# Kernel tuning notes

Measured on AMD Instinct MI355X. Metric: run time of the kernel, lower is better.

The kernel has to match this reference:

```python
import jax, jax.numpy as jnp
import numpy as np

B, D_IN, N, K, L, D_OUT = 64, 1024, 50000, 32, 3, 256


def setup_inputs() -> dict:
    key = jax.random.key(0)
    k = jax.random.split(key, 7)
    x = jax.random.normal(k[0], (B, D_IN), dtype=jnp.float32)
    W0 = jax.random.normal(k[1], (N, D_IN), dtype=jnp.float32) * 0.02
    b0 = jax.random.normal(k[2], (N,), dtype=jnp.float32) * 0.02
    Wv = jax.random.normal(k[3], (L, N, K), dtype=jnp.float32) * 0.1
    Wout = jax.random.normal(k[4], (D_OUT, N), dtype=jnp.float32) * 0.02
    bout = jax.random.normal(k[5], (D_OUT,), dtype=jnp.float32) * 0.02
    src = jax.random.randint(k[6], (L, N, K), 0, N, dtype=jnp.int64)
    return {"x": x, "W0": W0, "b0": b0, "Wv": Wv, "Wout": Wout, "bout": bout, "src": src}


def reference(x, W0, b0, Wv, Wout, bout, src):
    # layer 0: dense input->sources, relu, transpose -> [N, B]
    h = jax.nn.relu(x @ W0.T + b0).T

    # each hidden layer: per-vertex gather of K source activations + 1xK matmul + relu
    def step(h_prev, layer):
        w, s = layer                      # w: [N, K], s: [N, K]
        gathered = h_prev[s]              # [N, K, B] irregular gather
        h_new = jax.nn.relu(jnp.einsum('nk,nkb->nb', w, gathered))
        return h_new, None

    h, _ = jax.lax.scan(step, h, (Wv, src))

    # last layer -> output Linear (the module's _linear_dummy)
    return h.T @ Wout.T + bout            # [B, D_OUT]
```

## Files before the change

kernel.cpp:

```cpp
#include <hip/hip_runtime.h>

#define NV 50000
#define NVP 50176
#define BDIM 64
#define DIN 1024
#define KFAN 32
#define DOUT 256
#define KSTEPS (DIN / 32)
#define XPK_N (KSTEPS * 512)
#define OPC_CHUNK 128
#define OPC_NCH (NVP / OPC_CHUNK)

typedef short bf16x8 __attribute__((ext_vector_type(8)));
typedef float f32x4 __attribute__((ext_vector_type(4)));

__device__ __forceinline__ unsigned short bf16_rtn(float f) {
  unsigned u = __float_as_uint(f);
  return (unsigned short)((u + 0x7fffu + ((u >> 16) & 1u)) >> 16);
}
__device__ __forceinline__ float bf16_to_f(unsigned short v) {
  return __uint_as_float(((unsigned)v) << 16);
}
__device__ __forceinline__ void gload_lds16(const void* g, void* l) {
  __builtin_amdgcn_global_load_lds(
      (const __attribute__((address_space(1))) void*)g,
      (__attribute__((address_space(3))) void*)l, 16, 0, 0);
}

__global__ __launch_bounds__(256) void pack_x(const float* __restrict__ x,
                                              uint4* __restrict__ xpk8) {
  int tid = blockIdx.x * 256 + threadIdx.x;
  int ks = tid >> 8;
  int g = (tid >> 6) & 3;
  int l = tid & 63;
  int b = g * 16 + (l & 15);
  int k0 = ks * 32 + (l >> 4) * 8;
  unsigned hi[8], lo[8];
#pragma unroll
  for (int j = 0; j < 8; ++j) {
    float f = x[b * DIN + k0 + j];
    unsigned u = __float_as_uint(f);
    hi[j] = u >> 16;
    float fh = __uint_as_float(u & 0xffff0000u);
    lo[j] = bf16_rtn(f - fh);
  }
  uint4 vh, vl;
  vh.x = hi[0] | (hi[1] << 16); vh.y = hi[2] | (hi[3] << 16);
  vh.z = hi[4] | (hi[5] << 16); vh.w = hi[6] | (hi[7] << 16);
  vl.x = lo[0] | (lo[1] << 16); vl.y = lo[2] | (lo[3] << 16);
  vl.z = lo[4] | (lo[5] << 16); vl.w = lo[6] | (lo[7] << 16);
  int idx = (ks * 4 + g) * 128 + l;
#pragma unroll
  for (int c = 0; c < 8; ++c) {
    xpk8[(size_t)c * XPK_N + idx] = vh;
    xpk8[(size_t)c * XPK_N + idx + 64] = vl;
  }
}

__global__ __launch_bounds__(256) void layer0_mfma(
    const float* __restrict__ W0, const float* __restrict__ b0,
    const uint4* __restrict__ xpk8, unsigned short* __restrict__ h)
{
  __shared__ float wlds[2][64 * 32];
  __shared__ uint4 xlds[2][512];
  const int t = threadIdx.x;
  const int lane = t & 63;
  const int w = t >> 6;
  const int rq = lane >> 4;
  const int rr = lane & 15;
  const int n0 = blockIdx.x * 64;
  const uint4* xsrc = xpk8 + (size_t)(blockIdx.x & 7) * XPK_N;

  int s_row[2], s_srcg[2];
#pragma unroll
  for (int p = 0; p < 2; ++p) {
    int flat = p * 256 + t;
    s_row[p] = flat >> 3;
    s_srcg[p] = (flat & 7) ^ (s_row[p] & 7);
  }
  int rowg0 = n0 + s_row[0]; if (rowg0 > NV - 1) rowg0 = NV - 1;
  int rowg1 = n0 + s_row[1]; if (rowg1 > NV - 1) rowg1 = NV - 1;
  const float* sp0 = W0 + (size_t)rowg0 * DIN + s_srcg[0] * 4;
  const float* sp1 = W0 + (size_t)rowg1 * DIN + s_srcg[1] * 4;

  const int myrow = w * 16 + rr;
  const int sw = (myrow & 7) << 4;
  const int off0 = (myrow * 128 + ((rq * 32) ^ sw)) >> 2;
  const int off1 = (myrow * 128 + ((rq * 32 + 16) ^ sw)) >> 2;

  f32x4 acc[4];
#pragma unroll
  for (int g = 0; g < 4; ++g) acc[g] = (f32x4){0.f, 0.f, 0.f, 0.f};

  gload_lds16(sp0, &wlds[0][(0 * 256 + t) * 4]);
  gload_lds16(sp1, &wlds[0][(1 * 256 + t) * 4]);
  gload_lds16(xsrc + (0 * 256 + t), &xlds[0][0 * 256 + t]);
  gload_lds16(xsrc + (1 * 256 + t), &xlds[0][1 * 256 + t]);
  __syncthreads();

  for (int ks = 0; ks < KSTEPS; ++ks) {
    const int cur = ks & 1;
    if (ks + 1 < KSTEPS) {
      const int ko = (ks + 1) * 32;
      gload_lds16(sp0 + ko, &wlds[cur ^ 1][(0 * 256 + t) * 4]);
      gload_lds16(sp1 + ko, &wlds[cur ^ 1][(1 * 256 + t) * 4]);
      const uint4* xs = xsrc + (ks + 1) * 512;
      gload_lds16(xs + (0 * 256 + t), &xlds[cur ^ 1][0 * 256 + t]);
      gload_lds16(xs + (1 * 256 + t), &xlds[cur ^ 1][1 * 256 + t]);
    }
    uint4 xc[4][2];
#pragma unroll
    for (int g = 0; g < 4; ++g) {
      xc[g][0] = xlds[cur][g * 128 + lane];
      xc[g][1] = xlds[cur][g * 128 + 64 + lane];
    }
    const float* wb = &wlds[cur][0];
    float4 wv0 = *(const float4*)(wb + off0);
    float4 wv1 = *(const float4*)(wb + off1);
    bf16x8 whi, wlo;
    {
      float wf[8] = {wv0.x, wv0.y, wv0.z, wv0.w, wv1.x, wv1.y, wv1.z, wv1.w};
#pragma unroll
      for (int e = 0; e < 8; ++e) {
        unsigned u = __float_as_uint(wf[e]);
        whi[e] = (short)(u >> 16);
        float l = wf[e] - __uint_as_float(u & 0xffff0000u);
        wlo[e] = (short)bf16_rtn(l);
      }
    }
#pragma unroll
    for (int g = 0; g < 4; ++g) {
      bf16x8 xh = __builtin_bit_cast(bf16x8, xc[g][0]);
      bf16x8 xl = __builtin_bit_cast(bf16x8, xc[g][1]);
      acc[g] = __builtin_amdgcn_mfma_f32_16x16x32_bf16(whi, xh, acc[g], 0, 0, 0);
      acc[g] = __builtin_amdgcn_mfma_f32_16x16x32_bf16(wlo, xh, acc[g], 0, 0, 0);
      acc[g] = __builtin_amdgcn_mfma_f32_16x16x32_bf16(whi, xl, acc[g], 0, 0, 0);
    }
    __syncthreads();
  }

#pragma unroll
  for (int r = 0; r < 4; ++r) {
    int n = n0 + w * 16 + rq * 4 + r;
    if (n < NV) {
      float bias = b0[n];
#pragma unroll
      for (int g = 0; g < 4; ++g) {
        float v = fmaxf(acc[g][r] + bias, 0.f);
        h[(size_t)n * BDIM + g * 16 + rr] = bf16_rtn(v);
      }
    }
  }
}

__global__ __launch_bounds__(256) void sparse_layer(
    const unsigned short* __restrict__ hin, const float* __restrict__ wv,
    const int* __restrict__ src, unsigned short* __restrict__ hout)
{
  const int lane = threadIdx.x & 63;
  int n = blockIdx.x * 4 + (threadIdx.x >> 6);
  n = __builtin_amdgcn_readfirstlane(n);
  const float* wrow = wv + (size_t)n * KFAN;
  const int* srow = src + (size_t)n * KFAN;
  float acc = 0.f;
#pragma unroll
  for (int k = 0; k < KFAN; ++k) {
    int s = srow[k];
    float w = wrow[k];
    acc = fmaf(w, bf16_to_f(hin[(size_t)s * BDIM + lane]), acc);
  }
  hout[(size_t)n * BDIM + lane] = bf16_rtn(fmaxf(acc, 0.f));
}

__global__ __launch_bounds__(256) void transpose_h(
    const unsigned short* __restrict__ h, unsigned short* __restrict__ hT)
{
  const int lane = threadIdx.x & 63;
  const int wv = threadIdx.x >> 6;
  const int n0 = (blockIdx.x * 4 + wv) * 8;
  unsigned short v[8];
#pragma unroll
  for (int i = 0; i < 8; ++i) {
    int n = n0 + i;
    v[i] = (n < NV) ? h[(size_t)n * BDIM + lane] : (unsigned short)0;
  }
  uint4 o;
  o.x = v[0] | ((unsigned)v[1] << 16);
  o.y = v[2] | ((unsigned)v[3] << 16);
  o.z = v[4] | ((unsigned)v[5] << 16);
  o.w = v[6] | ((unsigned)v[7] << 16);
  *(uint4*)(hT + (size_t)lane * NVP + n0) = o;
}

__global__ __launch_bounds__(64) void out_partial_mfma(
    const unsigned short* __restrict__ hT, const float* __restrict__ Wout,
    float* __restrict__ part)
{
  const int lane = threadIdx.x;
  const int rq = lane >> 4;
  const int rr = lane & 15;
  const int dtile = blockIdx.x;
  const int chunk = blockIdx.y;

  f32x4 acc[4][4];
#pragma unroll
  for (int f = 0; f < 4; ++f)
#pragma unroll
    for (int g = 0; g < 4; ++g) acc[f][g] = (f32x4){0.f, 0.f, 0.f, 0.f};

#pragma unroll
  for (int ks = 0; ks < OPC_CHUNK / 32; ++ks) {
    const int n0 = chunk * OPC_CHUNK + ks * 32 + rq * 8;
    bf16x8 hb[4];
#pragma unroll
    for (int g = 0; g < 4; ++g)
      hb[g] = *(const bf16x8*)(hT + (size_t)(g * 16 + rr) * NVP + n0);
    int nb = n0 > (NV - 8) ? (NV - 8) : n0;
#pragma unroll
    for (int f = 0; f < 4; ++f) {
      const float* wp = Wout + (size_t)(dtile * 64 + f * 16 + rr) * NV + nb;
      float4 a0 = *(const float4*)(wp);
      float4 a1 = *(const float4*)(wp + 4);
      float wf[8] = {a0.x, a0.y, a0.z, a0.w, a1.x, a1.y, a1.z, a1.w};
      bf16x8 whi, wlo;
#pragma unroll
      for (int e = 0; e < 8; ++e) {
        unsigned u = __float_as_uint(wf[e]);
        whi[e] = (short)(u >> 16);
        float l = wf[e] - __uint_as_float(u & 0xffff0000u);
        wlo[e] = (short)bf16_rtn(l);
      }
#pragma unroll
      for (int g = 0; g < 4; ++g) {
        acc[f][g] = __builtin_amdgcn_mfma_f32_16x16x32_bf16(whi, hb[g], acc[f][g], 0, 0, 0);
        acc[f][g] = __builtin_amdgcn_mfma_f32_16x16x32_bf16(wlo, hb[g], acc[f][g], 0, 0, 0);
      }
    }
  }
  float* pbase = part + ((size_t)dtile * OPC_NCH + chunk) * 4096;
#pragma unroll
  for (int f = 0; f < 4; ++f)
#pragma unroll
    for (int g = 0; g < 4; ++g)
#pragma unroll
      for (int r = 0; r < 4; ++r)
        pbase[(f * 16 + rq * 4 + r) * 64 + g * 16 + rr] = acc[f][g][r];
}

__global__ __launch_bounds__(256) void out_reduce(
    const float* __restrict__ part, const float* __restrict__ bout,
    float* __restrict__ out)
{
  int tid = blockIdx.x * 256 + threadIdx.x;
  int b = tid & 63;
  int d = tid >> 6;
  int dtile = d >> 6;
  int dd = d & 63;
  float s = bout[d];
  for (int c = 0; c < OPC_NCH; ++c)
    s += part[((size_t)dtile * OPC_NCH + c) * 4096 + dd * 64 + b];
  out[(size_t)b * DOUT + d] = s;
}

extern "C" void kernel_launch(void* const* d_in, const int* in_sizes, int n_in,
                              void* d_out, int out_size, void* d_ws, size_t ws_size,
                              hipStream_t stream)
{
  const float* x    = (const float*)d_in[0];
  const float* W0   = (const float*)d_in[1];
  const float* b0   = (const float*)d_in[2];
  const float* Wv   = (const float*)d_in[3];
  const float* Wout = (const float*)d_in[4];
  const float* bout = (const float*)d_in[5];
  const int*   src  = (const int*)d_in[6];
  float* out = (float*)d_out;

  char* ws = (char*)d_ws;
  const size_t hbf = (size_t)NV * BDIM * 2;
  const size_t hTb = (size_t)NVP * BDIM * 2;
  const size_t xpkb = (size_t)8 * XPK_N * 16;
  unsigned short* hb0 = (unsigned short*)ws;
  unsigned short* hb1 = (unsigned short*)(ws + hbf);
  unsigned short* hT  = (unsigned short*)(ws + 2 * hbf);
  uint4* xpk8 = (uint4*)(ws + 2 * hbf + hTb);
  float* part = (float*)(ws + 2 * hbf + hTb + xpkb);

  pack_x<<<32, 256, 0, stream>>>(x, xpk8);
  layer0_mfma<<<(NV + 63) / 64, 256, 0, stream>>>(W0, b0, xpk8, hb0);

  const size_t lstride = (size_t)NV * KFAN;
  sparse_layer<<<NV / 4, 256, 0, stream>>>(hb0, Wv, src, hb1);
  sparse_layer<<<NV / 4, 256, 0, stream>>>(hb1, Wv + lstride, src + lstride, hb0);
  sparse_layer<<<NV / 4, 256, 0, stream>>>(hb0, Wv + 2 * lstride, src + 2 * lstride, hb1);

  transpose_h<<<NVP / 32, 256, 0, stream>>>(hb1, hT);
  out_partial_mfma<<<dim3(4, OPC_NCH), 64, 0, stream>>>(hT, Wout, part);
  out_reduce<<<(BDIM * DOUT) / 256, 256, 0, stream>>>(part, bout, out);
}
```

Measured before the change: 185.8 us.

## Triple-buffer layer0 LDS staging with partial vmcnt waits

Replaces the double-buffered global-to-LDS pipeline in the dense layer-0 MFMA kernel with a three-stage ring that prefetches two K-steps ahead. Each step waits only for the oldest batch of loads (vmcnt(4)) rather than draining all of them through __syncthreads, so global loads can stay in flight during compute. This uses more LDS, which may lower occupancy, and it depends on hand-written waitcnt and barrier placement being correct.

```diff
diff --git a/kernel.cpp b/kernel.cpp
--- a/kernel.cpp
+++ b/kernel.cpp
@@ -61,8 +61,8 @@
     const float* __restrict__ W0, const float* __restrict__ b0,
     const uint4* __restrict__ xpk8, unsigned short* __restrict__ h)
 {
-  __shared__ float wlds[2][64 * 32];
-  __shared__ uint4 xlds[2][512];
+  __shared__ float wlds[3][64 * 32];
+  __shared__ uint4 xlds[3][512];
   const int t = threadIdx.x;
   const int lane = t & 63;
   const int w = t >> 6;
@@ -88,31 +88,38 @@
   const int off0 = (myrow * 128 + ((rq * 32) ^ sw)) >> 2;
   const int off1 = (myrow * 128 + ((rq * 32 + 16) ^ sw)) >> 2;
 
+  auto stage = [&](int ks, int buf) {
+    const int ko = ks * 32;
+    gload_lds16(sp0 + ko, &wlds[buf][(0 * 256 + t) * 4]);
+    gload_lds16(sp1 + ko, &wlds[buf][(1 * 256 + t) * 4]);
+    const uint4* xs = xsrc + ks * 512;
+    gload_lds16(xs + (0 * 256 + t), &xlds[buf][0 * 256 + t]);
+    gload_lds16(xs + (1 * 256 + t), &xlds[buf][1 * 256 + t]);
+  };
+
   f32x4 acc[4];
 #pragma unroll
   for (int g = 0; g < 4; ++g) acc[g] = (f32x4){0.f, 0.f, 0.f, 0.f};
 
-  gload_lds16(sp0, &wlds[0][(0 * 256 + t) * 4]);
-  gload_lds16(sp1, &wlds[0][(1 * 256 + t) * 4]);
-  gload_lds16(xsrc + (0 * 256 + t), &xlds[0][0 * 256 + t]);
-  gload_lds16(xsrc + (1 * 256 + t), &xlds[0][1 * 256 + t]);
-  __syncthreads();
-
+  stage(0, 0);
+  stage(1, 1);
+  asm volatile("s_waitcnt vmcnt(4)" ::: "memory");
+  __builtin_amdgcn_sched_barrier(0);
+  __builtin_amdgcn_s_barrier();
+
+  int cur = 0;
   for (int ks = 0; ks < KSTEPS; ++ks) {
-    const int cur = ks & 1;
-    if (ks + 1 < KSTEPS) {
-      const int ko = (ks + 1) * 32;
-      gload_lds16(sp0 + ko, &wlds[cur ^ 1][(0 * 256 + t) * 4]);
-      gload_lds16(sp1 + ko, &wlds[cur ^ 1][(1 * 256 + t) * 4]);
-      const uint4* xs = xsrc + (ks + 1) * 512;
-      gload_lds16(xs + (0 * 256 + t), &xlds[cur ^ 1][0 * 256 + t]);
-      gload_lds16(xs + (1 * 256 + t), &xlds[cur ^ 1][1 * 256 + t]);
-    }
+    if (ks + 2 < KSTEPS) {
+      int nb = cur + 2; if (nb >= 3) nb -= 3;
+      stage(ks + 2, nb);
+      __builtin_amdgcn_sched_barrier(0);
+    }
+    const uint4* xb = &xlds[cur][0];
     uint4 xc[4][2];
 #pragma unroll
     for (int g = 0; g < 4; ++g) {
-      xc[g][0] = xlds[cur][g * 128 + lane];
-      xc[g][1] = xlds[cur][g * 128 + 64 + lane];
+      xc[g][0] = xb[g * 128 + lane];
+      xc[g][1] = xb[g * 128 + 64 + lane];
     }
     const float* wb = &wlds[cur][0];
     float4 wv0 = *(const float4*)(wb + off0);
@@ -136,7 +143,16 @@
       acc[g] = __builtin_amdgcn_mfma_f32_16x16x32_bf16(wlo, xh, acc[g], 0, 0, 0);
       acc[g] = __builtin_amdgcn_mfma_f32_16x16x32_bf16(whi, xl, acc[g], 0, 0, 0);
     }
-    __syncthreads();
+    if (ks + 2 < KSTEPS) {
+      asm volatile("s_waitcnt vmcnt(4)" ::: "memory");
+      __builtin_amdgcn_sched_barrier(0);
+      __builtin_amdgcn_s_barrier();
+    } else if (ks + 1 < KSTEPS) {
+      asm volatile("s_waitcnt vmcnt(0)" ::: "memory");
+      __builtin_amdgcn_sched_barrier(0);
+      __builtin_amdgcn_s_barrier();
+    }
+    cur = (cur == 2) ? 0 : cur + 1;
   }
 
 #pragma unroll
```

Measured after the change: 205.5 us. +10.6%, slower.

## Deepen layer-0 W0 staging to 128-column chunks and read x from global

Applied to the files above, without the earlier changes.

The layer-0 GEMM now stages W0 through LDS in larger 128-column chunks, eight per row tile, using a wider XOR swizzle. Loads are issued two stages ahead with explicit vmcnt waits and barriers, replacing the old per-32-column double buffer. The packed x operand is no longer copied into LDS; each wave reads it straight from global memory, relying on cache hits. This cuts the number of barriers and keeps more W0 bytes in flight, but uses more LDS per block, which can lower occupancy, and adds global-load latency for x inside the MFMA loop.

```diff
diff --git a/kernel.cpp b/kernel.cpp
--- a/kernel.cpp
+++ b/kernel.cpp
@@ -61,8 +61,7 @@
     const float* __restrict__ W0, const float* __restrict__ b0,
     const uint4* __restrict__ xpk8, unsigned short* __restrict__ h)
 {
-  __shared__ float wlds[2][64 * 32];
-  __shared__ uint4 xlds[2][512];
+  __shared__ float wlds[2][64 * 128];
   const int t = threadIdx.x;
   const int lane = t & 63;
   const int w = t >> 6;
@@ -71,72 +70,73 @@
   const int n0 = blockIdx.x * 64;
   const uint4* xsrc = xpk8 + (size_t)(blockIdx.x & 7) * XPK_N;
 
-  int s_row[2], s_srcg[2];
-#pragma unroll
-  for (int p = 0; p < 2; ++p) {
-    int flat = p * 256 + t;
-    s_row[p] = flat >> 3;
-    s_srcg[p] = (flat & 7) ^ (s_row[p] & 7);
-  }
-  int rowg0 = n0 + s_row[0]; if (rowg0 > NV - 1) rowg0 = NV - 1;
-  int rowg1 = n0 + s_row[1]; if (rowg1 > NV - 1) rowg1 = NV - 1;
-  const float* sp0 = W0 + (size_t)rowg0 * DIN + s_srcg[0] * 4;
-  const float* sp1 = W0 + (size_t)rowg1 * DIN + s_srcg[1] * 4;
+  const float* sp[8];
+#pragma unroll
+  for (int p = 0; p < 8; ++p) {
+    int f = p * 256 + t;
+    int row = f >> 5;
+    int su = (f & 31) ^ (row & 31);
+    int rg = n0 + row; if (rg > NV - 1) rg = NV - 1;
+    sp[p] = W0 + (size_t)rg * DIN + su * 4;
+  }
+  auto stage = [&](int ss, int buf) {
+    const int co = ss * 128;
+#pragma unroll
+    for (int p = 0; p < 8; ++p)
+      gload_lds16(sp[p] + co, &wlds[buf][(p * 256 + t) * 4]);
+  };
 
   const int myrow = w * 16 + rr;
-  const int sw = (myrow & 7) << 4;
-  const int off0 = (myrow * 128 + ((rq * 32) ^ sw)) >> 2;
-  const int off1 = (myrow * 128 + ((rq * 32 + 16) ^ sw)) >> 2;
+  const int rowbase = myrow * 128;
+  const int swz = myrow & 31;
 
   f32x4 acc[4];
 #pragma unroll
   for (int g = 0; g < 4; ++g) acc[g] = (f32x4){0.f, 0.f, 0.f, 0.f};
 
-  gload_lds16(sp0, &wlds[0][(0 * 256 + t) * 4]);
-  gload_lds16(sp1, &wlds[0][(1 * 256 + t) * 4]);
-  gload_lds16(xsrc + (0 * 256 + t), &xlds[0][0 * 256 + t]);
-  gload_lds16(xsrc + (1 * 256 + t), &xlds[0][1 * 256 + t]);
-  __syncthreads();
-
-  for (int ks = 0; ks < KSTEPS; ++ks) {
-    const int cur = ks & 1;
-    if (ks + 1 < KSTEPS) {
-      const int ko = (ks + 1) * 32;
-      gload_lds16(sp0 + ko, &wlds[cur ^ 1][(0 * 256 + t) * 4]);
-      gload_lds16(sp1 + ko, &wlds[cur ^ 1][(1 * 256 + t) * 4]);
-      const uint4* xs = xsrc + (ks + 1) * 512;
-      gload_lds16(xs + (0 * 256 + t), &xlds[cur ^ 1][0 * 256 + t]);
-      gload_lds16(xs + (1 * 256 + t), &xlds[cur ^ 1][1 * 256 + t]);
-    }
-    uint4 xc[4][2];
-#pragma unroll
-    for (int g = 0; g < 4; ++g) {
-      xc[g][0] = xlds[cur][g * 128 + lane];
-      xc[g][1] = xlds[cur][g * 128 + 64 + lane];
-    }
-    const float* wb = &wlds[cur][0];
-    float4 wv0 = *(const float4*)(wb + off0);
-    float4 wv1 = *(const float4*)(wb + off1);
-    bf16x8 whi, wlo;
-    {
-      float wf[8] = {wv0.x, wv0.y, wv0.z, wv0.w, wv1.x, wv1.y, wv1.z, wv1.w};
-#pragma unroll
-      for (int e = 0; e < 8; ++e) {
-        unsigned u = __float_as_uint(wf[e]);
-        whi[e] = (short)(u >> 16);
-        float l = wf[e] - __uint_as_float(u & 0xffff0000u);
-        wlo[e] = (short)bf16_rtn(l);
-      }
-    }
-#pragma unroll
-    for (int g = 0; g < 4; ++g) {
-      bf16x8 xh = __builtin_bit_cast(bf16x8, xc[g][0]);
-      bf16x8 xl = __builtin_bit_cast(bf16x8, xc[g][1]);
-      acc[g] = __builtin_amdgcn_mfma_f32_16x16x32_bf16(whi, xh, acc[g], 0, 0, 0);
-      acc[g] = __builtin_amdgcn_mfma_f32_16x16x32_bf16(wlo, xh, acc[g], 0, 0, 0);
-      acc[g] = __builtin_amdgcn_mfma_f32_16x16x32_bf16(whi, xl, acc[g], 0, 0, 0);
+  stage(0, 0);
+  stage(1, 1);
+  asm volatile("s_waitcnt vmcnt(8)" ::: "memory");
+  __builtin_amdgcn_sched_barrier(0);
+  __builtin_amdgcn_s_barrier();
+
+  for (int ss = 0; ss < 8; ++ss) {
+    const int cur = ss & 1;
+#pragma unroll
+    for (int kk = 0; kk < 4; ++kk) {
+      const int xb = (ss * 4 + kk) * 512;
+      uint4 xc[4][2];
+#pragma unroll
+      for (int g = 0; g < 4; ++g) {
+        xc[g][0] = xsrc[xb + g * 128 + lane];
+        xc[g][1] = xsrc[xb + g * 128 + 64 + lane];
+      }
+      const int u0 = kk * 8 + rq * 2;
+      const float* wb = &wlds[cur][0];
+      float4 wv0 = *(const float4*)(wb + rowbase + ((u0 ^ swz) << 2));
+      float4 wv1 = *(const float4*)(wb + rowbase + (((u0 + 1) ^ swz) << 2));
+      bf16x8 whi, wlo;
+      {
+        float wf[8] = {wv0.x, wv0.y, wv0.z, wv0.w, wv1.x, wv1.y, wv1.z, wv1.w};
+#pragma unroll
+        for (int e = 0; e < 8; ++e) {
+          unsigned u = __float_as_uint(wf[e]);
+          whi[e] = (short)(u >> 16);
+          float l = wf[e] - __uint_as_float(u & 0xffff0000u);
+          wlo[e] = (short)bf16_rtn(l);
+        }
+      }
+#pragma unroll
+      for (int g = 0; g < 4; ++g) {
+        bf16x8 xh = __builtin_bit_cast(bf16x8, xc[g][0]);
+        bf16x8 xl = __builtin_bit_cast(bf16x8, xc[g][1]);
+        acc[g] = __builtin_amdgcn_mfma_f32_16x16x32_bf16(whi, xh, acc[g], 0, 0, 0);
+        acc[g] = __builtin_amdgcn_mfma_f32_16x16x32_bf16(wlo, xh, acc[g], 0, 0, 0);
+        acc[g] = __builtin_amdgcn_mfma_f32_16x16x32_bf16(whi, xl, acc[g], 0, 0, 0);
+      }
     }
     __syncthreads();
+    if (ss + 2 < 8) stage(ss + 2, cur);
   }
 
 #pragma unroll
```

Result: slower. 202.9 us (+9.2%).
